# Optimization experiments

Hardware: AMD Instinct MI355X
Metric: run time of the kernel (lower is better)

The kernel has to match this reference:

```python
import jax, jax.numpy as jnp
import numpy as np

B, DIN, H = 16384, 512, 512
K = 7  # LC_i1, LC_i2, LC_f1, LC_f2, LC_o, LC_z (gate nets, idx 0..5), LC_d (decay net, idx 6)


def setup_inputs() -> dict:
    key = jax.random.key(0)
    ks = jax.random.split(key, 8)
    s1 = 1.0 / np.sqrt(DIN)
    s2 = 1.0 / np.sqrt(H)
    return {
        "hx": jax.random.normal(ks[0], (B, DIN), jnp.float32),
        "cx1": jax.random.normal(ks[1], (B, H), jnp.float32),
        "cx2": jax.random.normal(ks[2], (B, H), jnp.float32),
        # stacked params for the 7 sub-networks (same structure: Linear(DIN,H) -> Linear(H,H))
        "W1": jax.random.uniform(ks[3], (K, H, DIN), jnp.float32, -s1, s1),
        "b1": jax.random.uniform(ks[4], (K, H), jnp.float32, -s1, s1),
        "W2": jax.random.uniform(ks[5], (K, H, H), jnp.float32, -s2, s2),
        "b2": jax.random.uniform(ks[6], (K, H), jnp.float32, -s2, s2),
    }


def reference(hx, cx1, cx2, W1, b1, W2, b2):
    # layer 1 for all 7 nets at once: [K, B, H]
    h1 = jnp.einsum('bd,khd->kbh', hx, W1) + b1[:, None, :]
    # gate nets use tanh, decay net uses softplus
    a1 = jnp.concatenate([jnp.tanh(h1[:6]), jax.nn.softplus(h1[6:])], axis=0)
    # layer 2: [K, B, H]
    h2 = jnp.einsum('kbh,kgh->kbg', a1, W2) + b2[:, None, :]
    gates = jax.nn.sigmoid(jnp.tanh(h2[:6]))  # Gate_network: sigmoid(tanh(.))
    d = jax.nn.softplus(h2[6])                # Decay_network output (decay_coef, side state)
    i1, i2, f1, f2, o, zg = gates
    z = jnp.tanh(zg)                          # z = Tanh(LC_z(hx))
    cy1 = f1 * cx1 + i1 * z                   # side state self.cy1
    cy2 = f2 * cx2 + i2 * z
    return cy2
```

## Files before the change

kernel.cpp:

```cpp
#include <hip/hip_runtime.h>
#include <hip/hip_bf16.h>

typedef __attribute__((ext_vector_type(8))) __bf16 bf16x8;
typedef __attribute__((ext_vector_type(4))) __bf16 bf16x4;
typedef __attribute__((ext_vector_type(4))) float f32x4;

constexpr int M = 16384;
constexpr int K = 512;
constexpr int BK = 32;

__device__ __forceinline__ void async_copy16(const void* gsrc, void* ldst) {
  __builtin_amdgcn_global_load_lds(
      (const __attribute__((address_space(1))) unsigned int*)(gsrc),
      (__attribute__((address_space(3))) unsigned int*)(ldst),
      16, 0, 0);
}

__device__ __forceinline__ float frcp(float x) { return __builtin_amdgcn_rcpf(x); }
__device__ __forceinline__ float ftanh(float x) {
  return 1.0f - 2.0f * frcp(1.0f + __expf(2.0f * x));
}
__device__ __forceinline__ float fsigm(float x) { return frcp(1.0f + __expf(-x)); }

__device__ __forceinline__ int kswz(int row) {
  return ((row & 3) << 3) ^ ((row & 12) << 2);
}

template <int MODE>
__global__ __launch_bounds__(256) void gemm_kernel(
    const float* __restrict__ hx,
    const __bf16* __restrict__ Ab,
    const __bf16* __restrict__ W,
    const float* __restrict__ bias,
    __bf16* __restrict__ outb,
    const __bf16* __restrict__ gates,
    const float* __restrict__ cx2,
    float* __restrict__ outf)
{
  const int j = blockIdx.z;
  const int jj = (MODE == 3) ? 2 : j;
  const int mbase = blockIdx.x * 128;
  const int nbase = blockIdx.y * 128;
  constexpr size_t NH = (size_t)M * 512;

  const __bf16* Wj = W + (size_t)jj * 262144;
  const __bf16* Abj = (MODE >= 2) ? Ab + (size_t)jj * NH : nullptr;
  const int brow = 2 * jj + 1;

  __shared__ __align__(16) __bf16 smem[16384];

  const int tid  = threadIdx.x;
  const int wid  = tid >> 6;
  const int lane = tid & 63;
  const int wm   = (wid >> 1) * 64;
  const int wn   = (wid & 1) * 64;
  const int srow = wid * 16 + (lane >> 2);
  const int scol = ((lane & 3) ^ ((lane >> 3) & 3)) * 8;
  const int fr   = lane & 15;
  const int kc   = lane >> 4;
  const int sw   = (fr >> 1) & 3;
  const int rowq = kc * 4;

  const int ar = tid >> 1;
  const int cb = (tid & 1) * 2;
  const int asw = (ar >> 1) & 3;
  const float* hxrow =
      (MODE == 1) ? hx + (size_t)(mbase + ar) * K + cb * 8 : nullptr;

  auto stageW = [&](int p, int k0) {
    __bf16* As = smem + p * 8192;
    __bf16* Bs = As + 4096;
#pragma unroll
    for (int r = 0; r < 2; ++r)
      async_copy16(Wj + (size_t)(nbase + r * 64 + srow) * K + (k0 + scol),
                   (void*)&Bs[(r * 64 + wid * 16) * BK]);
    if constexpr (MODE >= 2) {
#pragma unroll
      for (int r = 0; r < 2; ++r)
        async_copy16(Abj + (size_t)(mbase + r * 64 + srow) * K + (k0 + scol),
                     (void*)&As[(r * 64 + wid * 16) * BK]);
    }
  };

  f32x4 av0, av1, av2, av3;
  auto loadA = [&](int k0) {
    const float* hp = hxrow + k0;
    av0 = *(const f32x4*)(hp);
    av1 = *(const f32x4*)(hp + 4);
    av2 = *(const f32x4*)(hp + 8);
    av3 = *(const f32x4*)(hp + 12);
  };
  auto writeA = [&](int p) {
    __bf16* As_ = smem + p * 8192 + ar * 32;
    *(bf16x4*)&As_[(cb ^ asw) * 8]           = __builtin_convertvector(av0, bf16x4);
    *(bf16x4*)&As_[(cb ^ asw) * 8 + 4]       = __builtin_convertvector(av1, bf16x4);
    *(bf16x4*)&As_[((cb + 1) ^ asw) * 8]     = __builtin_convertvector(av2, bf16x4);
    *(bf16x4*)&As_[((cb + 1) ^ asw) * 8 + 4] = __builtin_convertvector(av3, bf16x4);
  };

  f32x4 acc[4][4] = {};

  if constexpr (MODE == 1) {
    loadA(0);
    stageW(0, 0);
    writeA(0);
  } else {
    stageW(0, 0);
  }

  int p = 0;
  for (int k0 = 0; k0 < K; k0 += BK) {
    __syncthreads();
    const bool pre = k0 + BK < K;
    if (pre) {
      if constexpr (MODE == 1) loadA(k0 + BK);
      stageW(p ^ 1, k0 + BK);
    }

    const __bf16* As = smem + p * 8192;
    const __bf16* Bs = As + 4096;
    bf16x8 af[4], bfr[4];
#pragma unroll
    for (int i = 0; i < 4; ++i) {
      af[i]  = *(const bf16x8*)&As[(wm + i * 16 + fr) * BK + ((kc ^ sw) * 8)];
      bfr[i] = *(const bf16x8*)&Bs[(wn + i * 16 + fr) * BK + ((kc ^ sw) * 8)];
    }
#pragma unroll
    for (int mi = 0; mi < 4; ++mi)
#pragma unroll
      for (int ni = 0; ni < 4; ++ni)
        acc[mi][ni] = __builtin_amdgcn_mfma_f32_16x16x32_bf16(
            af[mi], bfr[ni], acc[mi][ni], 0, 0, 0);

    if constexpr (MODE == 1)
      if (pre) writeA(p ^ 1);
    p ^= 1;
  }

  float bv[4];
  const float* bj = bias + (size_t)brow * 512 + nbase + wn;
#pragma unroll
  for (int ni = 0; ni < 4; ++ni) bv[ni] = bj[ni * 16 + fr];

  __syncthreads();
#pragma unroll
  for (int mi = 0; mi < 4; ++mi)
#pragma unroll
    for (int ni = 0; ni < 4; ++ni)
#pragma unroll
      for (int r = 0; r < 4; ++r) {
        float v = acc[mi][ni][r] + bv[ni];
        float res;
        if constexpr (MODE == 1) res = ftanh(v);
        else if constexpr (MODE == 2) res = fsigm(ftanh(v));
        else res = ftanh(fsigm(ftanh(v)));
        const int row = wm + mi * 16 + rowq + r;
        const int col = wn + ni * 16 + fr;
        smem[row * 128 + (col ^ kswz(row))] = (__bf16)res;
      }
  __syncthreads();

  if constexpr (MODE <= 2) {
#pragma unroll
    for (int it = 0; it < 8; ++it) {
      const int s = it * 256 + tid;
      const int row = s >> 4, ch = s & 15;
      bf16x8 v = *(const bf16x8*)&smem[row * 128 + ((ch * 8) ^ kswz(row))];
      *(bf16x8*)&outb[(size_t)j * NH + (size_t)(mbase + row) * 512 +
                      (nbase + ch * 8)] = v;
    }
  } else {
#pragma unroll
    for (int it = 0; it < 8; ++it) {
      const int s = it * 256 + tid;
      const int row = s >> 4, ch = s & 15;
      const size_t gidx = (size_t)(mbase + row) * 512 + (nbase + ch * 8);
      bf16x8 zv = *(const bf16x8*)&smem[row * 128 + ((ch * 8) ^ kswz(row))];
      bf16x8 i2 = *(const bf16x8*)&gates[gidx];
      bf16x8 f2 = *(const bf16x8*)&gates[NH + gidx];
      f32x4 c0 = *(const f32x4*)&cx2[gidx];
      f32x4 c1 = *(const f32x4*)&cx2[gidx + 4];
      f32x4 r0, r1;
#pragma unroll
      for (int q = 0; q < 4; ++q) {
        r0[q] = (float)f2[q] * c0[q] + (float)i2[q] * (float)zv[q];
        r1[q] = (float)f2[4 + q] * c1[q] + (float)i2[4 + q] * (float)zv[4 + q];
      }
      *(f32x4*)&outf[gidx] = r0;
      *(f32x4*)&outf[gidx + 4] = r1;
    }
  }
}

__global__ __launch_bounds__(256) void cvt_w6(const float* __restrict__ W1,
                                              const float* __restrict__ W2,
                                              __bf16* __restrict__ dst) {
  const int y = blockIdx.y;
  const float* src = (y < 3) ? W1 + (size_t)(2 * y + 1) * 262144
                             : W2 + (size_t)(2 * (y - 3) + 1) * 262144;
  __bf16* d = dst + (size_t)y * 262144;
  const size_t i = ((size_t)blockIdx.x * 256 + threadIdx.x) * 4;
  f32x4 v = *(const f32x4*)&src[i];
  *(bf16x4*)&d[i] = __builtin_convertvector(v, bf16x4);
}

extern "C" void kernel_launch(void* const* d_in, const int* in_sizes, int n_in,
                              void* d_out, int out_size, void* d_ws, size_t ws_size,
                              hipStream_t stream) {
  const float* hx  = (const float*)d_in[0];
  const float* cx2 = (const float*)d_in[2];
  const float* W1  = (const float*)d_in[3];
  const float* b1  = (const float*)d_in[4];
  const float* W2  = (const float*)d_in[5];
  const float* b2  = (const float*)d_in[6];
  float* out = (float*)d_out;

  char* ws = (char*)d_ws;
  __bf16* W1b   = (__bf16*)(ws);
  __bf16* W2b   = (__bf16*)(ws + 1572864);
  __bf16* a1    = (__bf16*)(ws + 3145728);
  __bf16* gates = (__bf16*)(ws + 53477376);

  cvt_w6<<<dim3(256, 6), 256, 0, stream>>>(W1, W2, W1b);

  gemm_kernel<1><<<dim3(128, 4, 3), 256, 0, stream>>>(
      hx, nullptr, W1b, b1, a1, nullptr, nullptr, nullptr);
  gemm_kernel<2><<<dim3(128, 4, 2), 256, 0, stream>>>(
      nullptr, a1, W2b, b2, gates, nullptr, nullptr, nullptr);
  gemm_kernel<3><<<dim3(128, 4, 1), 256, 0, stream>>>(
      nullptr, a1, W2b, b2, nullptr, gates, cx2, out);
}
```

Baseline: 236.6 us.

## Pre-convert hx to bf16 and use 3-stage async LDS pipeline in GEMMs

hx is now converted to bf16 once in the combined conversion kernel, so layer 1 can stage both operands with async global-to-LDS copies like the other GEMMs. The GEMM main loop moves from double buffering with __syncthreads to a triple-buffered ring that prefetches two tiles ahead, using explicit vmcnt waits and raw barriers. The goal is to hide global load latency behind MFMA work. The cost is an extra 16 MB bf16 hx write and read, plus more LDS per block (48 KB), which may lower occupancy.

Result: faster. 224.1 us (-5.3%).

```diff
diff --git a/kernel.cpp b/kernel.cpp
--- a/kernel.cpp
+++ b/kernel.cpp
@@ -8,6 +8,7 @@
 constexpr int M = 16384;
 constexpr int K = 512;
 constexpr int BK = 32;
+constexpr int NT = 16;
 
 __device__ __forceinline__ void async_copy16(const void* gsrc, void* ldst) {
   __builtin_amdgcn_global_load_lds(
@@ -28,7 +29,6 @@
 
 template <int MODE>
 __global__ __launch_bounds__(256) void gemm_kernel(
-    const float* __restrict__ hx,
     const __bf16* __restrict__ Ab,
     const __bf16* __restrict__ W,
     const float* __restrict__ bias,
@@ -43,11 +43,11 @@
   const int nbase = blockIdx.y * 128;
   constexpr size_t NH = (size_t)M * 512;
 
+  const __bf16* Aj = (MODE == 1) ? Ab : Ab + (size_t)jj * NH;
   const __bf16* Wj = W + (size_t)jj * 262144;
-  const __bf16* Abj = (MODE >= 2) ? Ab + (size_t)jj * NH : nullptr;
   const int brow = 2 * jj + 1;
 
-  __shared__ __align__(16) __bf16 smem[16384];
+  __shared__ __align__(16) __bf16 smem[24576];
 
   const int tid  = threadIdx.x;
   const int wid  = tid >> 6;
@@ -61,63 +61,31 @@
   const int sw   = (fr >> 1) & 3;
   const int rowq = kc * 4;
 
-  const int ar = tid >> 1;
-  const int cb = (tid & 1) * 2;
-  const int asw = (ar >> 1) & 3;
-  const float* hxrow =
-      (MODE == 1) ? hx + (size_t)(mbase + ar) * K + cb * 8 : nullptr;
-
-  auto stageW = [&](int p, int k0) {
+  auto stage = [&](int p, int k0) {
     __bf16* As = smem + p * 8192;
     __bf16* Bs = As + 4096;
 #pragma unroll
-    for (int r = 0; r < 2; ++r)
+    for (int r = 0; r < 2; ++r) {
+      async_copy16(Aj + (size_t)(mbase + r * 64 + srow) * K + (k0 + scol),
+                   (void*)&As[(r * 64 + wid * 16) * BK]);
       async_copy16(Wj + (size_t)(nbase + r * 64 + srow) * K + (k0 + scol),
                    (void*)&Bs[(r * 64 + wid * 16) * BK]);
-    if constexpr (MODE >= 2) {
-#pragma unroll
-      for (int r = 0; r < 2; ++r)
-        async_copy16(Abj + (size_t)(mbase + r * 64 + srow) * K + (k0 + scol),
-                     (void*)&As[(r * 64 + wid * 16) * BK]);
     }
   };
 
-  f32x4 av0, av1, av2, av3;
-  auto loadA = [&](int k0) {
-    const float* hp = hxrow + k0;
-    av0 = *(const f32x4*)(hp);
-    av1 = *(const f32x4*)(hp + 4);
-    av2 = *(const f32x4*)(hp + 8);
-    av3 = *(const f32x4*)(hp + 12);
-  };
-  auto writeA = [&](int p) {
-    __bf16* As_ = smem + p * 8192 + ar * 32;
-    *(bf16x4*)&As_[(cb ^ asw) * 8]           = __builtin_convertvector(av0, bf16x4);
-    *(bf16x4*)&As_[(cb ^ asw) * 8 + 4]       = __builtin_convertvector(av1, bf16x4);
-    *(bf16x4*)&As_[((cb + 1) ^ asw) * 8]     = __builtin_convertvector(av2, bf16x4);
-    *(bf16x4*)&As_[((cb + 1) ^ asw) * 8 + 4] = __builtin_convertvector(av3, bf16x4);
-  };
-
   f32x4 acc[4][4] = {};
 
-  if constexpr (MODE == 1) {
-    loadA(0);
-    stageW(0, 0);
-    writeA(0);
-  } else {
-    stageW(0, 0);
-  }
-
-  int p = 0;
-  for (int k0 = 0; k0 < K; k0 += BK) {
-    __syncthreads();
-    const bool pre = k0 + BK < K;
-    if (pre) {
-      if constexpr (MODE == 1) loadA(k0 + BK);
-      stageW(p ^ 1, k0 + BK);
-    }
-
-    const __bf16* As = smem + p * 8192;
+  stage(0, 0);
+  stage(1, BK);
+  int pr = 0, ps = 2;
+  for (int t = 0; t < NT; ++t) {
+    if (t < NT - 2) asm volatile("s_waitcnt vmcnt(4) lgkmcnt(0)" ::: "memory");
+    else            asm volatile("s_waitcnt vmcnt(0) lgkmcnt(0)" ::: "memory");
+    __builtin_amdgcn_s_barrier();
+    __builtin_amdgcn_sched_barrier(0);
+    if (t < NT - 2) stage(ps, (t + 2) * BK);
+
+    const __bf16* As = smem + pr * 8192;
     const __bf16* Bs = As + 4096;
     bf16x8 af[4], bfr[4];
 #pragma unroll
@@ -132,9 +100,8 @@
         acc[mi][ni] = __builtin_amdgcn_mfma_f32_16x16x32_bf16(
             af[mi], bfr[ni], acc[mi][ni], 0, 0, 0);
 
-    if constexpr (MODE == 1)
-      if (pre) writeA(p ^ 1);
-    p ^= 1;
+    pr = (pr == 2) ? 0 : pr + 1;
+    ps = (ps == 2) ? 0 : ps + 1;
   }
 
   float bv[4];
@@ -192,16 +159,26 @@
   }
 }
 
-__global__ __launch_bounds__(256) void cvt_w6(const float* __restrict__ W1,
-                                              const float* __restrict__ W2,
-                                              __bf16* __restrict__ dst) {
-  const int y = blockIdx.y;
-  const float* src = (y < 3) ? W1 + (size_t)(2 * y + 1) * 262144
-                             : W2 + (size_t)(2 * (y - 3) + 1) * 262144;
-  __bf16* d = dst + (size_t)y * 262144;
-  const size_t i = ((size_t)blockIdx.x * 256 + threadIdx.x) * 4;
-  f32x4 v = *(const f32x4*)&src[i];
-  *(bf16x4*)&d[i] = __builtin_convertvector(v, bf16x4);
+__global__ __launch_bounds__(256) void cvt_all(const float* __restrict__ hx,
+                                               const float* __restrict__ W1,
+                                               const float* __restrict__ W2,
+                                               __bf16* __restrict__ hxb,
+                                               __bf16* __restrict__ Wb) {
+  const int b = blockIdx.x;
+  if (b < 1536) {
+    const int y = b >> 8;
+    const int bb = b & 255;
+    const float* src = (y < 3) ? W1 + (size_t)(2 * y + 1) * 262144
+                               : W2 + (size_t)(2 * (y - 3) + 1) * 262144;
+    __bf16* d = Wb + (size_t)y * 262144;
+    const size_t i = ((size_t)bb * 256 + threadIdx.x) * 4;
+    f32x4 v = *(const f32x4*)&src[i];
+    *(bf16x4*)&d[i] = __builtin_convertvector(v, bf16x4);
+  } else {
+    const size_t i = ((size_t)(b - 1536) * 256 + threadIdx.x) * 4;
+    f32x4 v = *(const f32x4*)&hx[i];
+    *(bf16x4*)&hxb[i] = __builtin_convertvector(v, bf16x4);
+  }
 }
 
 extern "C" void kernel_launch(void* const* d_in, const int* in_sizes, int n_in,
@@ -216,17 +193,18 @@
   float* out = (float*)d_out;
 
   char* ws = (char*)d_ws;
-  __bf16* W1b   = (__bf16*)(ws);
-  __bf16* W2b   = (__bf16*)(ws + 1572864);
-  __bf16* a1    = (__bf16*)(ws + 3145728);
-  __bf16* gates = (__bf16*)(ws + 53477376);
-
-  cvt_w6<<<dim3(256, 6), 256, 0, stream>>>(W1, W2, W1b);
+  __bf16* Wb    = (__bf16*)(ws);
+  __bf16* hxb   = (__bf16*)(ws + 3145728);
+  __bf16* a1    = (__bf16*)(ws + 19922944);
+  __bf16* gates = (__bf16*)(ws + 70254592);
+  __bf16* W2b   = Wb + 3 * 262144;
+
+  cvt_all<<<9728, 256, 0, stream>>>(hx, W1, W2, hxb, Wb);
 
   gemm_kernel<1><<<dim3(128, 4, 3), 256, 0, stream>>>(
-      hx, nullptr, W1b, b1, a1, nullptr, nullptr, nullptr);
+      hxb, Wb, b1, a1, nullptr, nullptr, nullptr);
   gemm_kernel<2><<<dim3(128, 4, 2), 256, 0, stream>>>(
-      nullptr, a1, W2b, b2, gates, nullptr, nullptr, nullptr);
+      a1, W2b, b2, gates, nullptr, nullptr, nullptr);
   gemm_kernel<3><<<dim3(128, 4, 1), 256, 0, stream>>>(
-      nullptr, a1, W2b, b2, nullptr, gates, cx2, out);
-}
+      a1, W2b, b2, nullptr, gates, cx2, out);
+}
```
